# Optimization experiments

Measured on AMD Instinct MI355X. Metric: run time of the kernel, lower is better.

Reference implementation:

```python
import jax, jax.numpy as jnp
import numpy as np

N_NODES = 50000
N_EDGES = 400000
F_IN = 70
E_DIM = 4
HID = 128
HEADS = 4


def _add_self_loops(src, dst, edge_attr, n):
    # PyG GATConv(add_self_loops=True, fill_value='mean' when edge_dim is set):
    # self-loop edge_attr = per-dst-node mean of incoming edge_attr.
    cnt = jax.ops.segment_sum(jnp.ones((src.shape[0],), edge_attr.dtype), dst, n)
    loop_attr = jax.ops.segment_sum(edge_attr, dst, n) / jnp.clip(cnt, 1.0)[:, None]
    loop = jnp.arange(n, dtype=src.dtype)
    return (jnp.concatenate([src, loop]), jnp.concatenate([dst, loop]),
            jnp.concatenate([edge_attr, loop_attr], axis=0))


def _gat_layer(x, src, dst, e_attr, W, a_src, a_dst, We, a_edge, b, concat):
    # W: [in, H*D]; a_src/a_dst/a_edge: [H, D]; We: [edge_dim, H*D]
    n = x.shape[0]
    H, D = a_src.shape
    xs = (x @ W).reshape(n, H, D)                      # [N,H,D]
    s_src = jnp.einsum('nhd,hd->nh', xs, a_src)        # [N,H]
    s_dst = jnp.einsum('nhd,hd->nh', xs, a_dst)
    ee = (e_attr @ We).reshape(-1, H, D)               # [E,H,D]
    s_edge = jnp.einsum('ehd,hd->eh', ee, a_edge)
    alpha = jax.nn.leaky_relu(s_src[src] + s_dst[dst] + s_edge, 0.2)  # [E,H]
    # segment softmax over edges grouped by destination node
    m = jax.ops.segment_max(alpha, dst, n)
    m = jnp.where(jnp.isfinite(m), m, 0.0)
    ex = jnp.exp(alpha - m[dst])
    denom = jax.ops.segment_sum(ex, dst, n)
    alpha = ex / (denom[dst] + 1e-16)
    msg = xs[src] * alpha[..., None]                   # [E,H,D] -- dominant traffic
    agg = jax.ops.segment_sum(msg, dst, n)             # [N,H,D]
    out = agg.reshape(n, H * D) if concat else agg.mean(axis=1)
    return out + b


def _layer_norm(x, g, b, eps=1e-5):
    mu = x.mean(-1, keepdims=True)
    var = ((x - mu) ** 2).mean(-1, keepdims=True)
    return (x - mu) * jax.lax.rsqrt(var + eps) * g + b


def setup_inputs() -> dict:
    key = jax.random.key(0)
    ks = jax.random.split(key, 24)
    f32 = jnp.float32
    node_features = jax.random.normal(ks[0], (N_NODES, F_IN), f32)
    edge_index = jax.random.randint(ks[1], (2, N_EDGES), 0, N_NODES, jnp.int32)
    edge_attr = jax.random.uniform(ks[2], (N_EDGES, E_DIM), f32)
    s = 0.1
    return {
        'node_features': node_features,
        'edge_index': edge_index,
        'edge_attr': edge_attr,
        'W1': jax.random.normal(ks[3], (F_IN, HEADS * HID), f32) * s,
        'as1': jax.random.normal(ks[4], (HEADS, HID), f32) * s,
        'ad1': jax.random.normal(ks[5], (HEADS, HID), f32) * s,
        'We1': jax.random.normal(ks[6], (E_DIM, HEADS * HID), f32) * s,
        'ae1': jax.random.normal(ks[7], (HEADS, HID), f32) * s,
        'b1': jnp.zeros((HEADS * HID,), f32),
        # GAT layer 2: 512 -> 128, 1 head, mean
        'W2': jax.random.normal(ks[8], (HEADS * HID, HID), f32) * s,
        'as2': jax.random.normal(ks[9], (1, HID), f32) * s,
        'ad2': jax.random.normal(ks[10], (1, HID), f32) * s,
        'We2': jax.random.normal(ks[11], (E_DIM, HID), f32) * s,
        'ae2': jax.random.normal(ks[12], (1, HID), f32) * s,
        'b2': jnp.zeros((HID,), f32),
        'ln_g': jnp.ones((HID,), f32),
        'ln_b': jnp.zeros((HID,), f32),
        'pw': jax.random.normal(ks[13], (HID, 8), f32) * s,
        'pb': jnp.zeros((8,), f32),
        'dw': jax.random.normal(ks[14], (HID, 4), f32) * s,
        'db': jnp.zeros((4,), f32),
    }


def reference(node_features, edge_index, edge_attr, W1, as1, ad1, We1, ae1, b1,
              W2, as2, ad2, We2, ae2, b2, ln_g, ln_b, pw, pb, dw, db):
    n = node_features.shape[0]
    src, dst, ea = _add_self_loops(edge_index[0], edge_index[1], edge_attr, n)
    x = jax.nn.gelu(_gat_layer(node_features, src, dst, ea, W1, as1, ad1, We1, ae1, b1, True), approximate=False)
    x = jax.nn.gelu(_gat_layer(x, src, dst, ea, W2, as2, ad2, We2, ae2, b2, False), approximate=False)
    x = _layer_norm(x, ln_g, ln_b)
    return (x @ pw + pb, x @ dw + db)
```

## Files before the change

kernel.cpp:

```cpp
#include <hip/hip_runtime.h>
#include <hip/hip_bf16.h>
#include <math.h>

#define NN 50000
#define NE 400000
#define FIN 70
#define EDIM 4
#define HIDD 128
#define NHEAD 4
constexpr int ET = NE + NN;
constexpr int KP1 = 96;
constexpr int NFP = 72;
constexpr int SCB = (NN + 255) / 256;

constexpr size_t al4(size_t x){ return (x + 3) & ~size_t(3); }
constexpr size_t CNT_O   = 0;
constexpr size_t ZEND    = al4(CNT_O + NN);
constexpr size_t CSR_O   = ZEND;
constexpr size_t BSUM_O  = al4(CSR_O + NN + 1);
constexpr size_t BOFF_O  = al4(BSUM_O + 256);
constexpr size_t EPK_O   = al4(BOFF_O + 256);
constexpr size_t EXF1_O  = al4(EPK_O + (size_t)ET*4);
constexpr size_t EXF2_O  = al4(EXF1_O + (size_t)ET*4);
constexpr size_t SS1_O   = al4(EXF2_O + ET);
constexpr size_t SD1_O   = al4(SS1_O + (size_t)NN*4);
constexpr size_t SS2_O   = al4(SD1_O + (size_t)NN*4);
constexpr size_t SD2_O   = al4(SS2_O + NN);
constexpr size_t CST_O   = al4(SD2_O + NN);
constexpr size_t W1T_O   = al4(CST_O + 2048);
constexpr size_t W2T_O   = al4(W1T_O + 4*128*KP1/2);
constexpr size_t NFB_O   = al4(W2T_O + 128*512/2);
constexpr size_t AGG_O   = al4(NFB_O + (size_t)NN*NFP/2);
constexpr size_t X1_O    = al4(AGG_O + (size_t)4*NN*KP1/2);
constexpr size_t XS2_O   = al4(X1_O + (size_t)NN*512/2);

constexpr int VS1 = 0;
constexpr int VD1 = 320;
constexpr int VE1 = 640;
constexpr int VE2 = 656;
constexpr int VS2 = 704;
constexpr int VD2 = 1216;

typedef short s8v __attribute__((ext_vector_type(8)));
typedef float f4v __attribute__((ext_vector_type(4)));

__device__ __forceinline__ unsigned short f2b(float v){
  __hip_bfloat16 b = __float2bfloat16(v);
  return *(unsigned short*)&b;
}
__device__ __forceinline__ float b2f(unsigned u_lo16){
  return __uint_as_float(u_lo16 << 16);
}
__device__ __forceinline__ unsigned pk2(float lo, float hi){
  return (unsigned)f2b(lo) | ((unsigned)f2b(hi) << 16);
}
__device__ __forceinline__ float lrelu(float x){ return x > 0.f ? x : 0.2f * x; }

__device__ __forceinline__ float gelu_fast(float x){
  float z = x * 0.70710678118654752440f;
  float a = fabsf(z);
  float t = 1.f / (1.f + 0.3275911f * a);
  float p = ((((1.061405429f*t - 1.453152027f)*t + 1.421413741f)*t
              - 0.284496736f)*t + 0.254829592f)*t;
  float erfv = 1.f - p * __expf(-a * a);
  erfv = copysignf(erfv, z);
  return 0.5f * x * (1.f + erfv);
}

__device__ __forceinline__ void gl16(const unsigned short* g, unsigned short* l){
  __builtin_amdgcn_global_load_lds(
      (const __attribute__((address_space(1))) unsigned int*)g,
      (__attribute__((address_space(3))) unsigned int*)l, 16, 0, 0);
}

__global__ void k_deg(const int* __restrict__ ei, int* __restrict__ cnt){
  int e = blockIdx.x * 256 + threadIdx.x;
  if (e >= NE) return;
  atomicAdd(&cnt[ei[NE + e]], 1);
}

__global__ void k_scan1(const int* __restrict__ cnt, int* __restrict__ bsum){
  __shared__ int ws[4];
  int t = threadIdx.x, lane = t & 63, w = t >> 6;
  int i = blockIdx.x * 256 + t;
  int v = (i < NN) ? cnt[i] + 1 : 0;
  for (int o = 32; o; o >>= 1) v += __shfl_down(v, o);
  if (lane == 0) ws[w] = v;
  __syncthreads();
  if (t == 0) bsum[blockIdx.x] = ws[0] + ws[1] + ws[2] + ws[3];
}

__global__ void k_scan2(const int* __restrict__ bsum, int* __restrict__ boff){
  __shared__ int ws[4];
  int t = threadIdx.x, lane = t & 63, w = t >> 6;
  int v = (t < SCB) ? bsum[t] : 0;
  int x = v;
  #pragma unroll
  for (int o = 1; o < 64; o <<= 1){ int u = __shfl_up(x, o); if (lane >= o) x += u; }
  if (lane == 63) ws[w] = x;
  __syncthreads();
  if (w == 0 && lane < 4){
    int y = ws[lane];
    #pragma unroll
    for (int o = 1; o < 4; o <<= 1){ int u = __shfl_up(y, o); if (lane >= o) y += u; }
    ws[lane] = y;
  }
  __syncthreads();
  int incl = x + (w > 0 ? ws[w - 1] : 0);
  if (t < SCB) boff[t] = incl - v;
}

__global__ void k_scan3(const int* __restrict__ cnt, const int* __restrict__ boff,
                        int* __restrict__ csr){
  __shared__ int ws[4];
  int t = threadIdx.x, lane = t & 63, w = t >> 6;
  int i = blockIdx.x * 256 + t;
  int v = (i < NN) ? cnt[i] + 1 : 0;
  int x = v;
  #pragma unroll
  for (int o = 1; o < 64; o <<= 1){ int u = __shfl_up(x, o); if (lane >= o) x += u; }
  if (lane == 63) ws[w] = x;
  __syncthreads();
  if (w == 0 && lane < 4){
    int y = ws[lane];
    #pragma unroll
    for (int o = 1; o < 4; o <<= 1){ int u = __shfl_up(y, o); if (lane >= o) y += u; }
    ws[lane] = y;
  }
  __syncthreads();
  if (i < NN) csr[i + 1] = boff[blockIdx.x] + (w > 0 ? ws[w - 1] : 0) + x;
  if (i == 0) csr[0] = 0;
}

__global__ void k_fill(const int* __restrict__ ei, const float* __restrict__ ea,
                       const int* __restrict__ csr, int* __restrict__ cnt,
                       int4* __restrict__ epk, const float* __restrict__ ss1,
                       const float* __restrict__ sd1, const float* __restrict__ C,
                       float4* __restrict__ exf){
  int e = blockIdx.x * 256 + threadIdx.x;
  if (e >= NE) return;
  int s = ei[e], d = ei[NE + e];
  int r = atomicSub(&cnt[d], 1);
  int p = csr[d] + r - 1;
  float4 a = *(const float4*)&ea[(size_t)e * 4];
  epk[p] = make_int4(s, d, (int)pk2(a.x, a.y), (int)pk2(a.z, a.w));
  float4 ssv = *(const float4*)&ss1[(size_t)s * 4];
  float4 sdv = *(const float4*)&sd1[(size_t)d * 4];
  float e0 = __expf(lrelu(ssv.x + sdv.x + a.x*C[VE1+0] + a.y*C[VE1+4] + a.z*C[VE1+8]  + a.w*C[VE1+12]));
  float e1 = __expf(lrelu(ssv.y + sdv.y + a.x*C[VE1+1] + a.y*C[VE1+5] + a.z*C[VE1+9]  + a.w*C[VE1+13]));
  float e2 = __expf(lrelu(ssv.z + sdv.z + a.x*C[VE1+2] + a.y*C[VE1+6] + a.z*C[VE1+10] + a.w*C[VE1+14]));
  float e3 = __expf(lrelu(ssv.w + sdv.w + a.x*C[VE1+3] + a.y*C[VE1+7] + a.z*C[VE1+11] + a.w*C[VE1+15]));
  exf[p] = make_float4(e0, e1, e2, e3);
}

__global__ void k_loopself(const int* __restrict__ csr, int4* __restrict__ epk,
                           const float* __restrict__ ss1, const float* __restrict__ sd1,
                           const float* __restrict__ C, float4* __restrict__ exf){
  int n = blockIdx.x * 256 + threadIdx.x;
  if (n >= NN) return;
  int a = csr[n], b = csr[n + 1];
  int deg = b - a - 1;
  float s0 = 0.f, s1 = 0.f, s2 = 0.f, s3 = 0.f;
  for (int p = a; p < b - 1; ++p){
    int4 v = epk[p];
    s0 += b2f((unsigned)v.z & 0xffffu); s1 += b2f((unsigned)v.z >> 16);
    s2 += b2f((unsigned)v.w & 0xffffu); s3 += b2f((unsigned)v.w >> 16);
  }
  float inv = 1.f / (float)(deg > 1 ? deg : 1);
  float m0 = s0*inv, m1 = s1*inv, m2 = s2*inv, m3 = s3*inv;
  epk[b - 1] = make_int4(n, n, (int)pk2(m0, m1), (int)pk2(m2, m3));
  float4 ssv = *(const float4*)&ss1[(size_t)n * 4];
  float4 sdv = *(const float4*)&sd1[(size_t)n * 4];
  float e0 = __expf(lrelu(ssv.x + sdv.x + m0*C[VE1+0] + m1*C[VE1+4] + m2*C[VE1+8]  + m3*C[VE1+12]));
  float e1 = __expf(lrelu(ssv.y + sdv.y + m0*C[VE1+1] + m1*C[VE1+5] + m2*C[VE1+9]  + m3*C[VE1+13]));
  float e2 = __expf(lrelu(ssv.z + sdv.z + m0*C[VE1+2] + m1*C[VE1+6] + m2*C[VE1+10] + m3*C[VE1+14]));
  float e3 = __expf(lrelu(ssv.w + sdv.w + m0*C[VE1+3] + m1*C[VE1+7] + m2*C[VE1+11] + m3*C[VE1+15]));
  exf[b - 1] = make_float4(e0, e1, e2, e3);
}

__global__ void k_prep(const float* __restrict__ W1, const float* __restrict__ as1,
                       const float* __restrict__ ad1, const float* __restrict__ We1,
                       const float* __restrict__ ae1, const float* __restrict__ W2,
                       const float* __restrict__ as2, const float* __restrict__ ad2,
                       const float* __restrict__ We2, const float* __restrict__ ae2,
                       float* __restrict__ C){
  int t = threadIdx.x;
  if (t < 280){
    int k = t >> 2, h = t & 3;
    float s = 0.f, d = 0.f;
    for (int dd = 0; dd < 128; ++dd){
      float w = W1[k*512 + h*128 + dd];
      s += w * as1[h*128 + dd];
      d += w * ad1[h*128 + dd];
    }
    C[VS1 + t] = s; C[VD1 + t] = d;
  }
  if (t < 16){
    int k = t >> 2, h = t & 3;
    float s = 0.f;
    for (int dd = 0; dd < 128; ++dd) s += We1[k*512 + h*128 + dd] * ae1[h*128 + dd];
    C[VE1 + t] = s;
  }
  if (t < 4){
    float s = 0.f;
    for (int dd = 0; dd < 128; ++dd) s += We2[t*128 + dd] * ae2[dd];
    C[VE2 + t] = s;
  }
  {
    float s = 0.f, d = 0.f;
    for (int dd = 0; dd < 128; ++dd){
      float w = W2[t*128 + dd];
      s += w * as2[dd];
      d += w * ad2[dd];
    }
    C[VS2 + t] = s; C[VD2 + t] = d;
  }
}

__global__ void k_tw(const float* __restrict__ W1, const float* __restrict__ W2,
                     unsigned short* __restrict__ W1t, unsigned short* __restrict__ W2t){
  int i = blockIdx.x * 256 + threadIdx.x;
  if (i < 4*128*KP1){
    int k = i % KP1, n = (i / KP1) & 127, h = i / (KP1*128);
    float v = (k < FIN) ? W1[k*512 + h*128 + n] : 0.f;
    W1t[i] = f2b(v);
  } else {
    int j = i - 4*128*KP1;
    if (j < 128*512){
      int k = j & 511, n = j >> 9;
      W2t[j] = f2b(W2[k*128 + n]);
    }
  }
}

__global__ __launch_bounds__(256) void k_cnfs1(const float* __restrict__ nf,
    const float* __restrict__ C, unsigned short* __restrict__ nfb,
    float* __restrict__ ss1, float* __restrict__ sd1){
  int lane = threadIdx.x & 63, w = threadIdx.x >> 6;
  int n = blockIdx.x * 4 + w;
  if (n >= NN) return;
  int c0 = lane * 2;
  bool act = lane < 35;
  float v0 = 0.f, v1 = 0.f;
  if (act){
    v0 = nf[(size_t)n * FIN + c0];
    v1 = nf[(size_t)n * FIN + c0 + 1];
  }
  if (lane < 36) *(unsigned*)&nfb[(size_t)n * NFP + c0] = act ? pk2(v0, v1) : 0u;
  float sh[4] = {0,0,0,0}, dh[4] = {0,0,0,0};
  if (act){
    float4 cs0 = *(const float4*)&C[VS1 + c0*4];
    float4 cs1 = *(const float4*)&C[VS1 + (c0+1)*4];
    float4 cd0 = *(const float4*)&C[VD1 + c0*4];
    float4 cd1 = *(const float4*)&C[VD1 + (c0+1)*4];
    sh[0] = v0*cs0.x + v1*cs1.x; sh[1] = v0*cs0.y + v1*cs1.y;
    sh[2] = v0*cs0.z + v1*cs1.z; sh[3] = v0*cs0.w + v1*cs1.w;
    dh[0] = v0*cd0.x + v1*cd1.x; dh[1] = v0*cd0.y + v1*cd1.y;
    dh[2] = v0*cd0.z + v1*cd1.z; dh[3] = v0*cd0.w + v1*cd1.w;
  }
  #pragma unroll
  for (int o = 32; o; o >>= 1){
    #pragma unroll
    for (int h = 0; h < 4; ++h){
      sh[h] += __shfl_xor(sh[h], o);
      dh[h] += __shfl_xor(dh[h], o);
    }
  }
  if (lane == 0){
    *(float4*)&ss1[(size_t)n*4] = make_float4(sh[0], sh[1], sh[2], sh[3]);
    *(float4*)&sd1[(size_t)n*4] = make_float4(dh[0], dh[1], dh[2], dh[3]);
  }
}

__global__ void k_al2(const int4* __restrict__ epk, const float* __restrict__ ss2,
                      const float* __restrict__ sd2, const float* __restrict__ C,
                      float* __restrict__ ex2){
  int p = blockIdx.x * 256 + threadIdx.x;
  if (p >= ET) return;
  int4 pk = epk[p];
  int s = pk.x, d = pk.y;
  float ax = b2f((unsigned)pk.z & 0xffffu), ay = b2f((unsigned)pk.z >> 16);
  float az = b2f((unsigned)pk.w & 0xffffu), aw = b2f((unsigned)pk.w >> 16);
  ex2[p] = __expf(lrelu(ss2[s] + sd2[d] +
             ax*C[VE2] + ay*C[VE2+1] + az*C[VE2+2] + aw*C[VE2+3]));
}

template<int MODE>
__global__ __launch_bounds__(256) void k_mfma(
    const unsigned short* __restrict__ A, int lda, long aSz,
    const unsigned short* __restrict__ Bt, long bSz,
    unsigned short* __restrict__ Cout, const float* __restrict__ bias,
    const float* __restrict__ Cv, float* __restrict__ ss2, float* __restrict__ sd2,
    int M, int KP){
  int z = blockIdx.y;
  A  += (size_t)z * aSz;
  Bt += (size_t)z * bSz;
  __shared__ unsigned short As[128 * 32];
  __shared__ unsigned short Bs[128 * 32];
  int tid = threadIdx.x, lane = tid & 63, w = tid >> 6;
  int wm = w & 1, wn = w >> 1;
  int row0 = blockIdx.x * 128;
  f4v acc[4][4] = {};
  int rl = lane >> 2, cslot = lane & 3;
  int m15 = lane & 15, j = lane >> 4;
  float s2a = 0.f, s2d = 0.f;
  int sr = tid >> 1, shf = tid & 1;
  int ssw = (sr ^ (sr >> 2)) & 3;
  for (int k0 = 0; k0 < KP; k0 += 32){
    #pragma unroll
    for (int half = 0; half < 2; ++half){
      int rb = w * 16 + half * 64;
      int r = rb + rl;
      int cs = cslot ^ ((r ^ (r >> 2)) & 3);
      int gr = row0 + r; if (gr >= M) gr = M - 1;
      gl16(A + (size_t)gr * lda + k0 + cs * 8, &As[rb * 32]);
      gl16(Bt + (size_t)r * lda + k0 + cs * 8, &Bs[rb * 32]);
    }
    __syncthreads();
    s8v af[4], bf[4];
    #pragma unroll
    for (int t = 0; t < 4; ++t){
      int ra = wm*64 + t*16 + m15;
      af[t] = *(const s8v*)&As[ra*32 + ((j ^ ((ra ^ (ra >> 2)) & 3)) * 8)];
      int rb2 = wn*64 + t*16 + m15;
      bf[t] = *(const s8v*)&Bs[rb2*32 + ((j ^ ((rb2 ^ (rb2 >> 2)) & 3)) * 8)];
    }
    if (MODE == 2){
      #pragma unroll
      for (int cc = 0; cc < 2; ++cc){
        int c = shf * 2 + cc;
        int kb = k0 + ((c ^ ssw) * 8);
        s8v xv = *(const s8v*)&As[sr*32 + c*8];
        #pragma unroll
        for (int t2 = 0; t2 < 8; ++t2){
          float xf = b2f((unsigned short)xv[t2]);
          s2a += xf * Cv[VS2 + kb + t2];
          s2d += xf * Cv[VD2 + kb + t2];
        }
      }
    }
    #pragma unroll
    for (int mi = 0; mi < 4; ++mi)
      #pragma unroll
      for (int ni = 0; ni < 4; ++ni)
        acc[mi][ni] = __builtin_amdgcn_mfma_f32_16x16x32_bf16(bf[ni], af[mi], acc[mi][ni], 0, 0, 0);
    __syncthreads();
  }
  int cq = lane & 15, rq = lane >> 4;
  #pragma unroll
  for (int mi = 0; mi < 4; ++mi){
    int grow = row0 + wm*64 + mi*16 + cq;
    if (grow < M){
      #pragma unroll
      for (int ni = 0; ni < 4; ++ni){
        int gc = wn*64 + ni*16 + rq*4;
        float v0 = acc[mi][ni][0], v1 = acc[mi][ni][1];
        float v2 = acc[mi][ni][2], v3 = acc[mi][ni][3];
        if (MODE == 1){
          float4 bv = *(const float4*)&bias[z*128 + gc];
          v0 = gelu_fast(v0 + bv.x); v1 = gelu_fast(v1 + bv.y);
          v2 = gelu_fast(v2 + bv.z); v3 = gelu_fast(v3 + bv.w);
          *(uint2*)&Cout[(size_t)grow*512 + z*128 + gc] = make_uint2(pk2(v0,v1), pk2(v2,v3));
        } else {
          *(uint2*)&Cout[(size_t)grow*128 + gc] = make_uint2(pk2(v0,v1), pk2(v2,v3));
        }
      }
    }
  }
  if (MODE == 2){
    float oa = s2a + __shfl_xor(s2a, 1);
    float od = s2d + __shfl_xor(s2d, 1);
    if (shf == 0){
      int grow = row0 + sr;
      if (grow < M){ ss2[grow] = oa; sd2[grow] = od; }
    }
  }
}

__global__ __launch_bounds__(256) void k_aggnf(const int* __restrict__ csr,
    const int4* __restrict__ epk, const float4* __restrict__ exf,
    const unsigned short* __restrict__ nfb, unsigned short* __restrict__ agg){
  int lane = threadIdx.x & 63, w = threadIdx.x >> 6;
  int n = blockIdx.x * 4 + w;
  if (n >= NN) return;
  int off = __builtin_amdgcn_readfirstlane(csr[n]);
  int end = __builtin_amdgcn_readfirstlane(csr[n + 1]);
  int col = lane * 2;
  bool act = lane < 36;
  float d0=0,d1=0,d2=0,d3=0;
  float a00=0,a01=0,a10=0,a11=0,a20=0,a21=0,a30=0,a31=0;
  int p = off;
  for (; p + 2 <= end; p += 2){
    int s0 = epk[p].x, s1 = epk[p+1].x;
    float4 e0 = exf[p], e1 = exf[p+1];
    unsigned u0 = 0, u1 = 0;
    if (act){
      u0 = *(const unsigned*)&nfb[(size_t)s0 * NFP + col];
      u1 = *(const unsigned*)&nfb[(size_t)s1 * NFP + col];
    }
    d0 += e0.x + e1.x; d1 += e0.y + e1.y; d2 += e0.z + e1.z; d3 += e0.w + e1.w;
    float v00 = b2f(u0 & 0xffffu), v01 = b2f(u0 >> 16);
    float v10 = b2f(u1 & 0xffffu), v11 = b2f(u1 >> 16);
    a00 += e0.x*v00 + e1.x*v10; a01 += e0.x*v01 + e1.x*v11;
    a10 += e0.y*v00 + e1.y*v10; a11 += e0.y*v01 + e1.y*v11;
    a20 += e0.z*v00 + e1.z*v10; a21 += e0.z*v01 + e1.z*v11;
    a30 += e0.w*v00 + e1.w*v10; a31 += e0.w*v01 + e1.w*v11;
  }
  if (p < end){
    int s0 = epk[p].x;
    float4 e0 = exf[p];
    unsigned u0 = 0;
    if (act) u0 = *(const unsigned*)&nfb[(size_t)s0 * NFP + col];
    d0 += e0.x; d1 += e0.y; d2 += e0.z; d3 += e0.w;
    float v00 = b2f(u0 & 0xffffu), v01 = b2f(u0 >> 16);
    a00 += e0.x*v00; a01 += e0.x*v01;
    a10 += e0.y*v00; a11 += e0.y*v01;
    a20 += e0.z*v00; a21 += e0.z*v01;
    a30 += e0.w*v00; a31 += e0.w*v01;
  }
  float i0 = 1.f/(d0+1e-16f), i1 = 1.f/(d1+1e-16f);
  float i2 = 1.f/(d2+1e-16f), i3 = 1.f/(d3+1e-16f);
  constexpr size_t HS = (size_t)NN * KP1;
  size_t base = (size_t)n * KP1 + col;
  if (act){
    *(unsigned*)&agg[base]        = pk2(a00*i0, a01*i0);
    *(unsigned*)&agg[base +   HS] = pk2(a10*i1, a11*i1);
    *(unsigned*)&agg[base + 2*HS] = pk2(a20*i2, a21*i2);
    *(unsigned*)&agg[base + 3*HS] = pk2(a30*i3, a31*i3);
  } else if (lane < 48){
    *(unsigned*)&agg[base]        = 0u;
    *(unsigned*)&agg[base +   HS] = 0u;
    *(unsigned*)&agg[base + 2*HS] = 0u;
    *(unsigned*)&agg[base + 3*HS] = 0u;
  }
}

__global__ __launch_bounds__(256) void k_agg2(
    const int* __restrict__ csr, const int4* __restrict__ epk,
    const float* __restrict__ ex2, const unsigned short* __restrict__ xs2b,
    const float* __restrict__ b2, const float* __restrict__ lng,
    const float* __restrict__ lnb, const float* __restrict__ pw,
    const float* __restrict__ pb, const float* __restrict__ dwm,
    const float* __restrict__ dbv, float* __restrict__ out){
  int lane = threadIdx.x & 63, w = threadIdx.x >> 6;
  int n = blockIdx.x * 4 + w;
  if (n >= NN) return;
  int off = __builtin_amdgcn_readfirstlane(csr[n]);
  int end = __builtin_amdgcn_readfirstlane(csr[n + 1]);
  int c0 = lane * 2;
  float acc0 = 0.f, acc1 = 0.f, den = 0.f;
  int p = off;
  for (; p + 4 <= end; p += 4){
    int s0 = epk[p].x, s1 = epk[p+1].x, s2 = epk[p+2].x, s3 = epk[p+3].x;
    float e0 = ex2[p], e1 = ex2[p+1], e2 = ex2[p+2], e3 = ex2[p+3];
    unsigned u0 = *(const unsigned*)&xs2b[(size_t)s0 * 128 + c0];
    unsigned u1 = *(const unsigned*)&xs2b[(size_t)s1 * 128 + c0];
    unsigned u2 = *(const unsigned*)&xs2b[(size_t)s2 * 128 + c0];
    unsigned u3 = *(const unsigned*)&xs2b[(size_t)s3 * 128 + c0];
    den += (e0 + e1) + (e2 + e3);
    acc0 += e0*b2f(u0 & 0xffffu) + e1*b2f(u1 & 0xffffu)
          + e2*b2f(u2 & 0xffffu) + e3*b2f(u3 & 0xffffu);
    acc1 += e0*b2f(u0 >> 16) + e1*b2f(u1 >> 16)
          + e2*b2f(u2 >> 16) + e3*b2f(u3 >> 16);
  }
  for (; p + 2 <= end; p += 2){
    int s0 = epk[p].x, s1 = epk[p+1].x;
    float e0 = ex2[p], e1 = ex2[p+1];
    unsigned u0 = *(const unsigned*)&xs2b[(size_t)s0 * 128 + c0];
    unsigned u1 = *(const unsigned*)&xs2b[(size_t)s1 * 128 + c0];
    den += e0 + e1;
    acc0 += e0*b2f(u0 & 0xffffu) + e1*b2f(u1 & 0xffffu);
    acc1 += e0*b2f(u0 >> 16) + e1*b2f(u1 >> 16);
  }
  if (p < end){
    int s0 = epk[p].x;
    float e0 = ex2[p];
    unsigned u0 = *(const unsigned*)&xs2b[(size_t)s0 * 128 + c0];
    den += e0;
    acc0 += e0*b2f(u0 & 0xffffu);
    acc1 += e0*b2f(u0 >> 16);
  }
  float invd = 1.f / (den + 1e-16f);
  float g0 = gelu_fast(acc0 * invd + b2[c0]);
  float g1 = gelu_fast(acc1 * invd + b2[c0 + 1]);
  float s = g0 + g1;
  #pragma unroll
  for (int o = 32; o; o >>= 1) s += __shfl_xor(s, o);
  float mu = s * (1.f / 128.f);
  float e0 = g0 - mu, e1 = g1 - mu;
  float q = e0*e0 + e1*e1;
  #pragma unroll
  for (int o = 32; o; o >>= 1) q += __shfl_xor(q, o);
  float rstd = rsqrtf(q * (1.f / 128.f) + 1e-5f);
  float y0 = e0 * rstd * lng[c0] + lnb[c0];
  float y1 = e1 * rstd * lng[c0 + 1] + lnb[c0 + 1];
  float pr[12];
  #pragma unroll
  for (int jj = 0; jj < 8; ++jj) pr[jj] = y0 * pw[c0*8 + jj] + y1 * pw[(c0+1)*8 + jj];
  #pragma unroll
  for (int jj = 0; jj < 4; ++jj) pr[8+jj] = y0 * dwm[c0*4 + jj] + y1 * dwm[(c0+1)*4 + jj];
  #pragma unroll
  for (int o = 32; o; o >>= 1)
    #pragma unroll
    for (int jj = 0; jj < 12; ++jj) pr[jj] += __shfl_xor(pr[jj], o);
  if (lane == 0){
    #pragma unroll
    for (int jj = 0; jj < 8; ++jj) out[(size_t)n*8 + jj] = pr[jj] + pb[jj];
    #pragma unroll
    for (int jj = 0; jj < 4; ++jj) out[(size_t)NN*8 + (size_t)n*4 + jj] = pr[8+jj] + dbv[jj];
  }
}

extern "C" void kernel_launch(void* const* d_in, const int* in_sizes, int n_in,
                              void* d_out, int out_size, void* d_ws, size_t ws_size,
                              hipStream_t stream){
  const float* nf  = (const float*)d_in[0];
  const int*   ei  = (const int*)  d_in[1];
  const float* ea  = (const float*)d_in[2];
  const float* W1  = (const float*)d_in[3];
  const float* as1 = (const float*)d_in[4];
  const float* ad1 = (const float*)d_in[5];
  const float* We1 = (const float*)d_in[6];
  const float* ae1 = (const float*)d_in[7];
  const float* b1  = (const float*)d_in[8];
  const float* W2  = (const float*)d_in[9];
  const float* as2 = (const float*)d_in[10];
  const float* ad2 = (const float*)d_in[11];
  const float* We2 = (const float*)d_in[12];
  const float* ae2 = (const float*)d_in[13];
  const float* b2  = (const float*)d_in[14];
  const float* lng = (const float*)d_in[15];
  const float* lnb = (const float*)d_in[16];
  const float* pw  = (const float*)d_in[17];
  const float* pb  = (const float*)d_in[18];
  const float* dw  = (const float*)d_in[19];
  const float* db  = (const float*)d_in[20];
  float* out = (float*)d_out;

  float* wf = (float*)d_ws;
  int*      cnt  = (int*)     (wf + CNT_O);
  int*      csr  = (int*)     (wf + CSR_O);
  int*      bsum = (int*)     (wf + BSUM_O);
  int*      boff = (int*)     (wf + BOFF_O);
  int4*     epk  = (int4*)    (wf + EPK_O);
  float4*   exf1 = (float4*)  (wf + EXF1_O);
  float*    ex2  =            (wf + EXF2_O);
  float*    ss1  =            (wf + SS1_O);
  float*    sd1  =            (wf + SD1_O);
  float*    ss2  =            (wf + SS2_O);
  float*    sd2  =            (wf + SD2_O);
  float*    Cc   =            (wf + CST_O);
  unsigned short* W1t = (unsigned short*)(wf + W1T_O);
  unsigned short* W2t = (unsigned short*)(wf + W2T_O);
  unsigned short* nfb = (unsigned short*)(wf + NFB_O);
  unsigned short* agg = (unsigned short*)(wf + AGG_O);
  unsigned short* x1  = (unsigned short*)(wf + X1_O);
  unsigned short* xs2b= (unsigned short*)(wf + XS2_O);

  hipMemsetAsync(cnt, 0, NN * sizeof(int), stream);
  k_prep<<<1, 512, 0, stream>>>(W1, as1, ad1, We1, ae1, W2, as2, ad2, We2, ae2, Cc);
  k_tw<<<(4*128*KP1 + 128*512 + 255) / 256, 256, 0, stream>>>(W1, W2, W1t, W2t);
  k_cnfs1<<<(NN + 3) / 4, 256, 0, stream>>>(nf, Cc, nfb, ss1, sd1);
  k_deg<<<(NE + 255) / 256, 256, 0, stream>>>(ei, cnt);
  k_scan1<<<SCB, 256, 0, stream>>>(cnt, bsum);
  k_scan2<<<1, 256, 0, stream>>>(bsum, boff);
  k_scan3<<<SCB, 256, 0, stream>>>(cnt, boff, csr);
  k_fill<<<(NE + 255) / 256, 256, 0, stream>>>(ei, ea, csr, cnt, epk, ss1, sd1, Cc, exf1);
  k_loopself<<<(NN + 255) / 256, 256, 0, stream>>>(csr, epk, ss1, sd1, Cc, exf1);
  k_aggnf<<<(NN + 3) / 4, 256, 0, stream>>>(csr, epk, exf1, nfb, agg);
  k_mfma<1><<<dim3((NN + 127) / 128, 4), 256, 0, stream>>>(
      agg, KP1, (long)NN * KP1, W1t, (long)128 * KP1, x1, b1,
      nullptr, nullptr, nullptr, NN, KP1);
  k_mfma<2><<<dim3((NN + 127) / 128, 1), 256, 0, stream>>>(
      x1, 512, 0, W2t, 0, xs2b, nullptr, Cc, ss2, sd2, NN, 512);
  k_al2<<<(ET + 255) / 256, 256, 0, stream>>>(epk, ss2, sd2, Cc, ex2);
  k_agg2<<<(NN + 3) / 4, 256, 0, stream>>>(csr, epk, ex2, xs2b,
                                           b2, lng, lnb, pw, pb, dw, db, out);
}
```

Measured before the change: 372.9 us.

## Fuse layer-1 and layer-2 GEMMs into one kernel keeping x1 in LDS

Replaces the two k_mfma launches with a single k_gemm12 kernel. Each block handles 32 rows: it computes the four per-head layer-1 GEMMs with bias and GELU, keeps the 32x512 bf16 x1 tile in shared memory, then multiplies it by W2 and computes the ss2/sd2 scores. This removes the write and re-read of the N x 512 intermediate x1 from global memory. In exchange it uses smaller 32-row tiles with more redundant weight loading, plain loads instead of global_load_lds, and larger LDS use that may lower occupancy.

```diff
diff --git a/kernel.cpp b/kernel.cpp
--- a/kernel.cpp
+++ b/kernel.cpp
@@ -31,8 +31,7 @@
 constexpr size_t W2T_O   = al4(W1T_O + 4*128*KP1/2);
 constexpr size_t NFB_O   = al4(W2T_O + 128*512/2);
 constexpr size_t AGG_O   = al4(NFB_O + (size_t)NN*NFP/2);
-constexpr size_t X1_O    = al4(AGG_O + (size_t)4*NN*KP1/2);
-constexpr size_t XS2_O   = al4(X1_O + (size_t)NN*512/2);
+constexpr size_t XS2_O   = al4(AGG_O + (size_t)4*NN*KP1/2);
 
 constexpr int VS1 = 0;
 constexpr int VD1 = 320;
@@ -65,12 +64,6 @@
   float erfv = 1.f - p * __expf(-a * a);
   erfv = copysignf(erfv, z);
   return 0.5f * x * (1.f + erfv);
-}
-
-__device__ __forceinline__ void gl16(const unsigned short* g, unsigned short* l){
-  __builtin_amdgcn_global_load_lds(
-      (const __attribute__((address_space(1))) unsigned int*)g,
-      (__attribute__((address_space(3))) unsigned int*)l, 16, 0, 0);
 }
 
 __global__ void k_deg(const int* __restrict__ ei, int* __restrict__ cnt){
@@ -285,96 +278,99 @@
              ax*C[VE2] + ay*C[VE2+1] + az*C[VE2+2] + aw*C[VE2+3]));
 }
 
-template<int MODE>
-__global__ __launch_bounds__(256) void k_mfma(
-    const unsigned short* __restrict__ A, int lda, long aSz,
-    const unsigned short* __restrict__ Bt, long bSz,
-    unsigned short* __restrict__ Cout, const float* __restrict__ bias,
-    const float* __restrict__ Cv, float* __restrict__ ss2, float* __restrict__ sd2,
-    int M, int KP){
-  int z = blockIdx.y;
-  A  += (size_t)z * aSz;
-  Bt += (size_t)z * bSz;
-  __shared__ unsigned short As[128 * 32];
-  __shared__ unsigned short Bs[128 * 32];
+__global__ __launch_bounds__(256) void k_gemm12(
+    const unsigned short* __restrict__ agg, const unsigned short* __restrict__ W1t,
+    const unsigned short* __restrict__ W2t, const float* __restrict__ b1,
+    const float* __restrict__ Cv, unsigned short* __restrict__ xs2b,
+    float* __restrict__ ss2, float* __restrict__ sd2){
+  __shared__ unsigned short xt[32 * 520];
+  __shared__ unsigned short Bs[128 * 40];
+  __shared__ unsigned short As[32 * 40];
   int tid = threadIdx.x, lane = tid & 63, w = tid >> 6;
   int wm = w & 1, wn = w >> 1;
-  int row0 = blockIdx.x * 128;
-  f4v acc[4][4] = {};
-  int rl = lane >> 2, cslot = lane & 3;
-  int m15 = lane & 15, j = lane >> 4;
-  float s2a = 0.f, s2d = 0.f;
-  int sr = tid >> 1, shf = tid & 1;
-  int ssw = (sr ^ (sr >> 2)) & 3;
-  for (int k0 = 0; k0 < KP; k0 += 32){
-    #pragma unroll
-    for (int half = 0; half < 2; ++half){
-      int rb = w * 16 + half * 64;
-      int r = rb + rl;
-      int cs = cslot ^ ((r ^ (r >> 2)) & 3);
-      int gr = row0 + r; if (gr >= M) gr = M - 1;
-      gl16(A + (size_t)gr * lda + k0 + cs * 8, &As[rb * 32]);
-      gl16(Bt + (size_t)r * lda + k0 + cs * 8, &Bs[rb * 32]);
-    }
-    __syncthreads();
-    s8v af[4], bf[4];
-    #pragma unroll
-    for (int t = 0; t < 4; ++t){
-      int ra = wm*64 + t*16 + m15;
-      af[t] = *(const s8v*)&As[ra*32 + ((j ^ ((ra ^ (ra >> 2)) & 3)) * 8)];
-      int rb2 = wn*64 + t*16 + m15;
-      bf[t] = *(const s8v*)&Bs[rb2*32 + ((j ^ ((rb2 ^ (rb2 >> 2)) & 3)) * 8)];
-    }
-    if (MODE == 2){
+  int m15 = lane & 15, rq = lane >> 4;
+  int r0 = blockIdx.x * 32;
+  constexpr size_t HS = (size_t)NN * KP1;
+  for (int h = 0; h < 4; ++h){
+    f4v acc[4] = {};
+    const unsigned short* Ah = agg + (size_t)h * HS;
+    const unsigned short* Wh = W1t + h * 128 * KP1;
+    for (int k0 = 0; k0 < KP1; k0 += 32){
+      if (tid < 128){
+        int r = tid >> 2, c = tid & 3;
+        int gr = r0 + r; if (gr >= NN) gr = NN - 1;
+        *(uint4*)&As[r*40 + c*8] = *(const uint4*)&Ah[(size_t)gr*KP1 + k0 + c*8];
+      }
       #pragma unroll
-      for (int cc = 0; cc < 2; ++cc){
-        int c = shf * 2 + cc;
-        int kb = k0 + ((c ^ ssw) * 8);
-        s8v xv = *(const s8v*)&As[sr*32 + c*8];
-        #pragma unroll
-        for (int t2 = 0; t2 < 8; ++t2){
-          float xf = b2f((unsigned short)xv[t2]);
-          s2a += xf * Cv[VS2 + kb + t2];
-          s2d += xf * Cv[VD2 + kb + t2];
-        }
+      for (int i = 0; i < 2; ++i){
+        int idx = tid + i*256;
+        int r = idx >> 2, c = idx & 3;
+        *(uint4*)&Bs[r*40 + c*8] = *(const uint4*)&Wh[r*KP1 + k0 + c*8];
       }
-    }
-    #pragma unroll
-    for (int mi = 0; mi < 4; ++mi)
-      #pragma unroll
-      for (int ni = 0; ni < 4; ++ni)
-        acc[mi][ni] = __builtin_amdgcn_mfma_f32_16x16x32_bf16(bf[ni], af[mi], acc[mi][ni], 0, 0, 0);
-    __syncthreads();
-  }
-  int cq = lane & 15, rq = lane >> 4;
-  #pragma unroll
-  for (int mi = 0; mi < 4; ++mi){
-    int grow = row0 + wm*64 + mi*16 + cq;
-    if (grow < M){
+      __syncthreads();
+      s8v af = *(const s8v*)&As[(wm*16 + m15)*40 + rq*8];
       #pragma unroll
       for (int ni = 0; ni < 4; ++ni){
-        int gc = wn*64 + ni*16 + rq*4;
-        float v0 = acc[mi][ni][0], v1 = acc[mi][ni][1];
-        float v2 = acc[mi][ni][2], v3 = acc[mi][ni][3];
-        if (MODE == 1){
-          float4 bv = *(const float4*)&bias[z*128 + gc];
-          v0 = gelu_fast(v0 + bv.x); v1 = gelu_fast(v1 + bv.y);
-          v2 = gelu_fast(v2 + bv.z); v3 = gelu_fast(v3 + bv.w);
-          *(uint2*)&Cout[(size_t)grow*512 + z*128 + gc] = make_uint2(pk2(v0,v1), pk2(v2,v3));
-        } else {
-          *(uint2*)&Cout[(size_t)grow*128 + gc] = make_uint2(pk2(v0,v1), pk2(v2,v3));
-        }
+        s8v bf = *(const s8v*)&Bs[(wn*64 + ni*16 + m15)*40 + rq*8];
+        acc[ni] = __builtin_amdgcn_mfma_f32_16x16x32_bf16(bf, af, acc[ni], 0, 0, 0);
       }
-    }
-  }
-  if (MODE == 2){
-    float oa = s2a + __shfl_xor(s2a, 1);
-    float od = s2d + __shfl_xor(s2d, 1);
-    if (shf == 0){
-      int grow = row0 + sr;
-      if (grow < M){ ss2[grow] = oa; sd2[grow] = od; }
-    }
-  }
+      __syncthreads();
+    }
+    int lr = wm*16 + m15;
+    #pragma unroll
+    for (int ni = 0; ni < 4; ++ni){
+      int cb = h*128 + wn*64 + ni*16 + rq*4;
+      float4 bv = *(const float4*)&b1[cb];
+      float v0 = gelu_fast(acc[ni][0] + bv.x);
+      float v1 = gelu_fast(acc[ni][1] + bv.y);
+      float v2 = gelu_fast(acc[ni][2] + bv.z);
+      float v3 = gelu_fast(acc[ni][3] + bv.w);
+      *(uint2*)&xt[lr*520 + cb] = make_uint2(pk2(v0,v1), pk2(v2,v3));
+    }
+  }
+  f4v acc2[4] = {};
+  for (int k0 = 0; k0 < 512; k0 += 32){
+    #pragma unroll
+    for (int i = 0; i < 2; ++i){
+      int idx = tid + i*256;
+      int r = idx >> 2, c = idx & 3;
+      *(uint4*)&Bs[r*40 + c*8] = *(const uint4*)&W2t[r*512 + k0 + c*8];
+    }
+    __syncthreads();
+    s8v af = *(const s8v*)&xt[(wm*16 + m15)*520 + k0 + rq*8];
+    #pragma unroll
+    for (int ni = 0; ni < 4; ++ni){
+      s8v bf = *(const s8v*)&Bs[(wn*64 + ni*16 + m15)*40 + rq*8];
+      acc2[ni] = __builtin_amdgcn_mfma_f32_16x16x32_bf16(bf, af, acc2[ni], 0, 0, 0);
+    }
+    __syncthreads();
+  }
+  int grow = r0 + wm*16 + m15;
+  if (grow < NN){
+    #pragma unroll
+    for (int ni = 0; ni < 4; ++ni){
+      int gc = wn*64 + ni*16 + rq*4;
+      *(uint2*)&xs2b[(size_t)grow*128 + gc] =
+          make_uint2(pk2(acc2[ni][0], acc2[ni][1]), pk2(acc2[ni][2], acc2[ni][3]));
+    }
+  }
+  int row = tid >> 3, ch = tid & 7;
+  float sa = 0.f, sdv = 0.f;
+  #pragma unroll
+  for (int jj = 0; jj < 8; ++jj){
+    int j2 = (jj + ch) & 7;
+    int cb = ch*64 + j2*8;
+    s8v xv = *(const s8v*)&xt[row*520 + cb];
+    #pragma unroll
+    for (int t2 = 0; t2 < 8; ++t2){
+      float xf = b2f((unsigned short)xv[t2]);
+      sa  += xf * Cv[VS2 + cb + t2];
+      sdv += xf * Cv[VD2 + cb + t2];
+    }
+  }
+  #pragma unroll
+  for (int o = 1; o < 8; o <<= 1){ sa += __shfl_xor(sa, o); sdv += __shfl_xor(sdv, o); }
+  if (ch == 0 && r0 + row < NN){ ss2[r0 + row] = sa; sd2[r0 + row] = sdv; }
 }
 
 __global__ __launch_bounds__(256) void k_aggnf(const int* __restrict__ csr,
@@ -554,7 +550,6 @@
   unsigned short* W2t = (unsigned short*)(wf + W2T_O);
   unsigned short* nfb = (unsigned short*)(wf + NFB_O);
   unsigned short* agg = (unsigned short*)(wf + AGG_O);
-  unsigned short* x1  = (unsigned short*)(wf + X1_O);
   unsigned short* xs2b= (unsigned short*)(wf + XS2_O);
 
   hipMemsetAsync(cnt, 0, NN * sizeof(int), stream);
@@ -568,11 +563,7 @@
   k_fill<<<(NE + 255) / 256, 256, 0, stream>>>(ei, ea, csr, cnt, epk, ss1, sd1, Cc, exf1);
   k_loopself<<<(NN + 255) / 256, 256, 0, stream>>>(csr, epk, ss1, sd1, Cc, exf1);
   k_aggnf<<<(NN + 3) / 4, 256, 0, stream>>>(csr, epk, exf1, nfb, agg);
-  k_mfma<1><<<dim3((NN + 127) / 128, 4), 256, 0, stream>>>(
-      agg, KP1, (long)NN * KP1, W1t, (long)128 * KP1, x1, b1,
-      nullptr, nullptr, nullptr, NN, KP1);
-  k_mfma<2><<<dim3((NN + 127) / 128, 1), 256, 0, stream>>>(
-      x1, 512, 0, W2t, 0, xs2b, nullptr, Cc, ss2, sd2, NN, 512);
+  k_gemm12<<<(NN + 31) / 32, 256, 0, stream>>>(agg, W1t, W2t, b1, Cc, xs2b, ss2, sd2);
   k_al2<<<(ET + 255) / 256, 256, 0, stream>>>(epk, ss2, sd2, Cc, ex2);
   k_agg2<<<(NN + 3) / 4, 256, 0, stream>>>(csr, epk, ex2, xs2b,
                                            b2, lng, lnb, pw, pb, dw, db, out);
```

New measurement: 372.4 us. Within noise of the previous version (-0.1%).
